# Optimization experiments

Measured on AMD Instinct MI355X. Metric: run time of the kernel, lower is better.

Reference implementation:

```python
import jax, jax.numpy as jnp
import numpy as np

DIM, SEQ, HEADS = 1024, 2048, 8
HEAD_DIM = DIM // HEADS


def setup_inputs() -> dict:
    key = jax.random.key(0)
    ks = jax.random.split(key, 8)
    x = jax.random.normal(ks[0], (4, SEQ, DIM), dtype=jnp.float32)
    # Linear weights stored [in, out]; y = x @ W + b (same math as torch Linear).
    Wk = jax.random.normal(ks[1], (DIM, DIM), dtype=jnp.float32) * (DIM ** -0.5)
    bk = jnp.zeros((DIM,), dtype=jnp.float32)
    Wv = jax.random.normal(ks[2], (DIM, DIM), dtype=jnp.float32) * (DIM ** -0.5)
    bv = jnp.zeros((DIM,), dtype=jnp.float32)
    # learned AFT position bias [heads, seq, seq]; small scale keeps exp stable
    w_aft = jax.random.normal(ks[3], (HEADS, SEQ, SEQ), dtype=jnp.float32) * 0.1
    Wo = jax.random.normal(ks[4], (DIM, DIM), dtype=jnp.float32) * (DIM ** -0.5)
    bo = jnp.zeros((DIM,), dtype=jnp.float32)
    return {"x": x, "Wk": Wk, "bk": bk, "Wv": Wv, "bv": bv,
            "w_aft": w_aft, "Wo": Wo, "bo": bo}


def reference(x, Wk, bk, Wv, bv, w_aft, Wo, bo):
    N, S, _ = x.shape
    k = (x @ Wk + bk).reshape(N, S, HEADS, HEAD_DIM)
    v = (x @ Wv + bv).reshape(N, S, HEADS, HEAD_DIM)
    ek = jnp.exp(k)  # [N,S,H,D]
    # causal mask: position t attends to i <= t; exp(w+k) = exp(w)*exp(k)
    causal = jnp.tril(jnp.ones((S, S), dtype=bool))
    ew = jnp.where(causal[None, :, :], jnp.exp(w_aft), 0.0)  # [H,T,S]
    num = jnp.einsum('hts,nshd->nthd', ew, ek * v)  # [N,T,H,D]
    den = jnp.einsum('hts,nshd->nthd', ew, ek)      # [N,T,H,D]
    aft = (num / den).reshape(N, S, DIM)
    return aft @ Wo + bo
```

## Files before the change

### kernel.cpp

```cpp
#include <hip/hip_runtime.h>
#include <hip/hip_bf16.h>
#include <stdint.h>

#define DIM 1024
#define SEQ 2048
#define NB 4
#define HEADS 8
#define HD 128
#define ROWS (NB*SEQ)

typedef __attribute__((ext_vector_type(8))) short bf16x8;
typedef __attribute__((ext_vector_type(4))) float f32x4;

#define VMCNT(n) asm volatile("s_waitcnt vmcnt(" #n ")" ::: "memory")
#define SBAR()   __builtin_amdgcn_s_barrier()
#define SCHED0() __builtin_amdgcn_sched_barrier(0)

static __device__ __forceinline__ unsigned short f2bf(float f){
  union { float f; unsigned int u; } x; x.f = f;
  unsigned int r = x.u + 0x7fffu + ((x.u >> 16) & 1u);
  return (unsigned short)(r >> 16);
}

static __device__ __forceinline__ void gld_lds16(const void* g, void* l){
  __builtin_amdgcn_global_load_lds(
      (const __attribute__((address_space(1))) void*)g,
      (__attribute__((address_space(3))) void*)l,
      16, 0, 0);
}

__global__ void k_prep(const float* __restrict__ x,
                       const float* __restrict__ Wk, const float* __restrict__ Wv,
                       const float* __restrict__ Wo, const float* __restrict__ waft,
                       unsigned short* __restrict__ xb,
                       unsigned short* __restrict__ Tk, unsigned short* __restrict__ Tv,
                       unsigned short* __restrict__ To, unsigned short* __restrict__ ewb){
  __shared__ float tile[64][65];
  const int B = blockIdx.x;
  const int tid = threadIdx.x;
  if (B < 2048){
    for (int i = B*256 + tid; i < ROWS*DIM/4; i += 2048*256){
      const float4 v = reinterpret_cast<const float4*>(x)[i];
      ushort4 o;
      o.x = f2bf(v.x); o.y = f2bf(v.y); o.z = f2bf(v.z); o.w = f2bf(v.w);
      reinterpret_cast<ushort4*>(xb)[i] = o;
    }
  } else if (B < 2816){
    const int D = B - 2048;
    const int z = D >> 8;
    const int rem = D & 255;
    const int bo = (rem & 15) * 64;
    const int bi = (rem >> 4) * 64;
    const float* W = (z == 0) ? Wk : (z == 1) ? Wv : Wo;
    unsigned short* WT = (z == 0) ? Tk : (z == 1) ? Tv : To;
    #pragma unroll
    for (int it = 0; it < 16; ++it){
      int f = it*256 + tid;
      int r = f >> 6, c = f & 63;
      tile[r][c] = W[(size_t)(bi + r) * DIM + bo + c];
    }
    __syncthreads();
    #pragma unroll
    for (int it = 0; it < 16; ++it){
      int f = it*256 + tid;
      int r = f >> 6, c = f & 63;
      WT[(size_t)(bo + r) * DIM + bi + c] = f2bf(tile[c][r]);
    }
  } else {
    const int D = B - 2816;
    const int t = D & 2047;
    const int h = D >> 11;
    const float* src = waft + ((size_t)h*SEQ + t) * SEQ;
    unsigned short* dst = ewb + ((size_t)h*SEQ + t) * SEQ;
    const int smax4 = ((t & ~127) + 128) >> 2;
    for (int i = tid; i < smax4; i += 256){
      const float4 w4 = reinterpret_cast<const float4*>(src)[i];
      const int s = i * 4;
      ushort4 o;
      o.x = (s+0 <= t) ? f2bf(__expf(w4.x)) : (unsigned short)0;
      o.y = (s+1 <= t) ? f2bf(__expf(w4.y)) : (unsigned short)0;
      o.z = (s+2 <= t) ? f2bf(__expf(w4.z)) : (unsigned short)0;
      o.w = (s+3 <= t) ? f2bf(__expf(w4.w)) : (unsigned short)0;
      reinterpret_cast<ushort4*>(dst)[i] = o;
    }
  }
}

__global__ __launch_bounds__(512) void k_proj(
    const unsigned short* __restrict__ xb,
    const unsigned short* __restrict__ wkt,
    const unsigned short* __restrict__ wvt,
    const float* __restrict__ bk,
    const float* __restrict__ bv,
    unsigned short* __restrict__ ekb)
{
  __shared__ __align__(16) char smem[131072];
  unsigned short* Asl = (unsigned short*)smem;
  unsigned short* Bsl = (unsigned short*)(smem + 65536);
  float* xch = (float*)smem;

  const int tid  = threadIdx.x;
  const int lane = tid & 63;
  const int lo   = lane & 15;
  const int hi   = lane >> 4;
  const int wid  = tid >> 6;
  const int wm   = wid >> 2;
  const int wn   = wid & 3;
  const int D    = blockIdx.x;
  const int mb   = D >> 3;
  const int cb   = D & 7;
  const int row0 = mb * 256;
  const int col0k = cb * 128;

  f32x4 acc[8][4] = {};

  auto stage_unit = [&](int kt, int slot, int u){
    const int half = u & 1;
    const bool isB = (u >> 1) != 0;
    unsigned short* lb = (isB ? Bsl : Asl) + slot*(256*64) + half*(128*64);
    const unsigned short* gb;
    if (!isB)           gb = xb  + (size_t)(row0 + half*128)*DIM + kt*64;
    else if (half == 0) gb = wkt + (size_t)col0k*DIM + kt*64;
    else                gb = wvt + (size_t)col0k*DIM + kt*64;
    #pragma unroll
    for (int it = 0; it < 2; ++it){
      const int po = (it*512 + tid)*16;
      const int r  = po >> 7;
      const int k2 = (po & 127) ^ ((r & 7) << 4);
      gld_lds16(gb + (size_t)r*DIM + (k2 >> 1), (char*)lb + po);
    }
  };

  #pragma unroll
  for (int u = 0; u < 4; ++u) stage_unit(0, 0, u);

  for (int t = 0; t < 16; ++t){
    const int s = t & 1;
    const char* Ab = (const char*)(Asl + s*(256*64));
    const char* Bb = (const char*)(Bsl + s*(256*64));
    #pragma unroll
    for (int q = 0; q < 4; ++q){
      if (t + 1 < 16) stage_unit(t + 1, s ^ 1, q);
      if (q == 0){
        if (t + 1 < 16) { VMCNT(2); } else { VMCNT(0); }
      }
      SCHED0();
      SBAR();
      SCHED0();
      bf16x8 a[2][2], b[4][2];
      #pragma unroll
      for (int mf = 0; mf < 2; ++mf){
        const int R = wm*128 + (q*2 + mf)*16 + lo;
        #pragma unroll
        for (int ks = 0; ks < 2; ++ks){
          const int K2 = (ks*64 + hi*16) ^ ((R & 7) << 4);
          a[mf][ks] = *reinterpret_cast<const bf16x8*>(Ab + R*128 + K2);
        }
      }
      #pragma unroll
      for (int nf = 0; nf < 4; ++nf){
        const int R = wn*64 + nf*16 + lo;
        #pragma unroll
        for (int ks = 0; ks < 2; ++ks){
          const int K2 = (ks*64 + hi*16) ^ ((R & 7) << 4);
          b[nf][ks] = *reinterpret_cast<const bf16x8*>(Bb + R*128 + K2);
        }
      }
      __builtin_amdgcn_s_setprio(1);
      #pragma unroll
      for (int ks = 0; ks < 2; ++ks)
        #pragma unroll
        for (int mf = 0; mf < 2; ++mf)
          #pragma unroll
          for (int nf = 0; nf < 4; ++nf)
            acc[q*2+mf][nf] = __builtin_amdgcn_mfma_f32_16x16x32_bf16(
                a[mf][ks], b[nf][ks], acc[q*2+mf][nf], 0, 0, 0);
      __builtin_amdgcn_s_setprio(0);
      SCHED0();
      SBAR();
    }
  }

  __syncthreads();
  if (wn >= 2){
    #pragma unroll
    for (int mf = 0; mf < 8; ++mf){
      const int rloc = wm*128 + mf*16 + hi*4;
      #pragma unroll
      for (int nf = 0; nf < 4; ++nf){
        const int cv = (wn - 2)*64 + nf*16 + lo;
        #pragma unroll
        for (int jj = 0; jj < 4; ++jj)
          xch[(size_t)(rloc + jj)*128 + cv] = acc[mf][nf][jj];
      }
    }
  }
  __syncthreads();
  if (wn < 2){
    #pragma unroll
    for (int nf = 0; nf < 4; ++nf){
      const int ck = wn*64 + nf*16 + lo;
      const int c  = col0k + ck;
      const int h  = c >> 7;
      const int d  = c & 127;
      const float bkc = bk[c];
      const float bvc = bv[c];
      #pragma unroll
      for (int mf = 0; mf < 8; ++mf){
        const int rloc = wm*128 + mf*16 + hi*4;
        const int r = row0 + rloc;
        const int n = r >> 11;
        const int sidx = r & 2047;
        ushort4 pk, pv;
        #pragma unroll
        for (int jj = 0; jj < 4; ++jj){
          const float kval = acc[mf][nf][jj] + bkc;
          const float vval = xch[(size_t)(rloc + jj)*128 + ck] + bvc;
          const float ek = __expf(kval);
          ((unsigned short*)&pk)[jj] = f2bf(ek);
          ((unsigned short*)&pv)[jj] = f2bf(ek * vval);
        }
        const size_t idx = ((size_t)h*1024 + n*256 + d) * SEQ + sidx;
        *reinterpret_cast<ushort4*>(&ekb[idx]) = pk;
        *reinterpret_cast<ushort4*>(&ekb[idx + (size_t)128*SEQ]) = pv;
      }
    }
  }
}

__global__ __launch_bounds__(512) void k_core(
    const unsigned short* __restrict__ ewb,
    const unsigned short* __restrict__ ekb,
    unsigned short* __restrict__ aftb)
{
  __shared__ __align__(16) char smem[98304];
  unsigned short* Asl = (unsigned short*)smem;
  unsigned short* Bsl = (unsigned short*)(smem + 32768);
  float* xch = (float*)smem;

  const int tid  = threadIdx.x;
  const int lane = tid & 63;
  const int lo   = lane & 15;
  const int hi   = lane >> 4;
  const int wid  = tid >> 6;
  const int wm   = wid >> 2;
  const int wn   = wid & 3;
  const int D  = blockIdx.x;
  const int h  = D & 7;
  const int r_ = D >> 3;
  const int p  = r_ >> 2;
  const int n  = r_ & 3;

  const unsigned short* slab = ekb + ((size_t)h*1024 + n*256) * SEQ;

  #pragma unroll
  for (int half = 0; half < 2; ++half){
    const int tt = half ? p : (15 - p);
    const int t0 = tt * 128;
    const int nst = 2*tt + 2;
    const unsigned short* abase = ewb + ((size_t)h*SEQ + t0) * SEQ;

    f32x4 acc[4][4] = {};

    auto stage_unit = [&](int st, int slot, int u){
      const int s0 = st * 64;
      const int po = tid * 16;
      const int r  = po >> 7;
      const int k2 = (po & 127) ^ ((r & 7) << 4);
      if (u < 2){
        unsigned short* lb = Asl + slot*(128*64) + u*(64*64);
        gld_lds16(abase + (size_t)(u*64 + r)*SEQ + s0 + (k2 >> 1), (char*)lb + po);
      } else {
        unsigned short* lb = Bsl + slot*(256*64) + (u-2)*(64*64);
        gld_lds16(slab + (size_t)((u-2)*64 + r)*SEQ + s0 + (k2 >> 1), (char*)lb + po);
      }
    };

    #pragma unroll
    for (int u = 0; u < 6; ++u) stage_unit(0, 0, u);

    for (int t = 0; t < nst; ++t){
      const int s = t & 1;
      const char* Ab = (const char*)(Asl + s*(128*64));
      const char* Bb = (const char*)(Bsl + s*(256*64));
      #pragma unroll
      for (int q = 0; q < 4; ++q){
        if (q < 3 && t + 1 < nst){
          stage_unit(t + 1, s ^ 1, q*2);
          stage_unit(t + 1, s ^ 1, q*2 + 1);
        }
        if (q == 0){
          if (t + 1 < nst) { VMCNT(2); } else { VMCNT(0); }
        }
        SCHED0();
        SBAR();
        SCHED0();
        bf16x8 a[2], b[4][2];
        {
          const int R = wm*64 + q*16 + lo;
          #pragma unroll
          for (int ks = 0; ks < 2; ++ks){
            const int K2 = (ks*64 + hi*16) ^ ((R & 7) << 4);
            a[ks] = *reinterpret_cast<const bf16x8*>(Ab + R*128 + K2);
          }
        }
        #pragma unroll
        for (int nf = 0; nf < 4; ++nf){
          const int R = wn*64 + nf*16 + lo;
          #pragma unroll
          for (int ks = 0; ks < 2; ++ks){
            const int K2 = (ks*64 + hi*16) ^ ((R & 7) << 4);
            b[nf][ks] = *reinterpret_cast<const bf16x8*>(Bb + R*128 + K2);
          }
        }
        __builtin_amdgcn_s_setprio(1);
        #pragma unroll
        for (int ks = 0; ks < 2; ++ks)
          #pragma unroll
          for (int nf = 0; nf < 4; ++nf)
            acc[q][nf] = __builtin_amdgcn_mfma_f32_16x16x32_bf16(
                a[ks], b[nf][ks], acc[q][nf], 0, 0, 0);
        __builtin_amdgcn_s_setprio(0);
        SCHED0();
        SBAR();
      }
    }

    __syncthreads();
    if (wn >= 2){
      #pragma unroll
      for (int mf = 0; mf < 4; ++mf){
        const int rloc = wm*64 + mf*16 + hi*4;
        #pragma unroll
        for (int nf = 0; nf < 4; ++nf){
          const int dv = (wn - 2)*64 + nf*16 + lo;
          #pragma unroll
          for (int jj = 0; jj < 4; ++jj)
            xch[(size_t)(rloc + jj)*129 + dv] = acc[mf][nf][jj];
        }
      }
    }
    __syncthreads();
    if (wn < 2){
      #pragma unroll
      for (int nf = 0; nf < 4; ++nf){
        const int d = wn*64 + nf*16 + lo;
        #pragma unroll
        for (int mf = 0; mf < 4; ++mf){
          const int rloc = wm*64 + mf*16 + hi*4;
          #pragma unroll
          for (int jj = 0; jj < 4; ++jj){
            const int t = t0 + rloc + jj;
            const float num = xch[(size_t)(rloc + jj)*129 + d];
            aftb[((size_t)n*SEQ + t)*DIM + h*HD + d] = f2bf(num / acc[mf][nf][jj]);
          }
        }
      }
    }
    __syncthreads();
  }
}

__global__ __launch_bounds__(512) void k_out(
    const unsigned short* __restrict__ aftb,
    const unsigned short* __restrict__ wot,
    const float* __restrict__ bo,
    float* __restrict__ out)
{
  __shared__ __align__(16) char smem[98304];
  unsigned short* Asl = (unsigned short*)smem;
  unsigned short* Bsl = (unsigned short*)(smem + 32768);

  const int tid  = threadIdx.x;
  const int lane = tid & 63;
  const int lo   = lane & 15;
  const int hi   = lane >> 4;
  const int wid  = tid >> 6;
  const int wm   = wid >> 2;
  const int wn   = wid & 3;
  const int D    = blockIdx.x;
  const int row0 = (D >> 2) * 128;
  const int col0 = (D & 3) * 256;

  f32x4 acc[4][4] = {};

  auto stage_unit = [&](int kt, int slot, int u){
    const int po = tid * 16;
    const int r  = po >> 7;
    const int k2 = (po & 127) ^ ((r & 7) << 4);
    if (u < 2){
      unsigned short* lb = Asl + slot*(128*64) + u*(64*64);
      gld_lds16(aftb + (size_t)(row0 + u*64 + r)*DIM + kt*64 + (k2 >> 1), (char*)lb + po);
    } else {
      unsigned short* lb = Bsl + slot*(256*64) + (u-2)*(64*64);
      gld_lds16(wot + (size_t)(col0 + (u-2)*64 + r)*DIM + kt*64 + (k2 >> 1), (char*)lb + po);
    }
  };

  #pragma unroll
  for (int u = 0; u < 6; ++u) stage_unit(0, 0, u);

  for (int t = 0; t < 16; ++t){
    const int s = t & 1;
    const char* Ab = (const char*)(Asl + s*(128*64));
    const char* Bb = (const char*)(Bsl + s*(256*64));
    #pragma unroll
    for (int q = 0; q < 4; ++q){
      if (q < 3 && t + 1 < 16){
        stage_unit(t + 1, s ^ 1, q*2);
        stage_unit(t + 1, s ^ 1, q*2 + 1);
      }
      if (q == 0){
        if (t + 1 < 16) { VMCNT(2); } else { VMCNT(0); }
      }
      SCHED0();
      SBAR();
      SCHED0();
      bf16x8 a[2], b[4][2];
      {
        const int R = wm*64 + q*16 + lo;
        #pragma unroll
        for (int ks = 0; ks < 2; ++ks){
          const int K2 = (ks*64 + hi*16) ^ ((R & 7) << 4);
          a[ks] = *reinterpret_cast<const bf16x8*>(Ab + R*128 + K2);
        }
      }
      #pragma unroll
      for (int nf = 0; nf < 4; ++nf){
        const int R = wn*64 + nf*16 + lo;
        #pragma unroll
        for (int ks = 0; ks < 2; ++ks){
          const int K2 = (ks*64 + hi*16) ^ ((R & 7) << 4);
          b[nf][ks] = *reinterpret_cast<const bf16x8*>(Bb + R*128 + K2);
        }
      }
      __builtin_amdgcn_s_setprio(1);
      #pragma unroll
      for (int ks = 0; ks < 2; ++ks)
        #pragma unroll
        for (int nf = 0; nf < 4; ++nf)
          acc[q][nf] = __builtin_amdgcn_mfma_f32_16x16x32_bf16(
              a[ks], b[nf][ks], acc[q][nf], 0, 0, 0);
      __builtin_amdgcn_s_setprio(0);
      SCHED0();
      SBAR();
    }
  }

  #pragma unroll
  for (int nf = 0; nf < 4; ++nf){
    const int c = col0 + wn*64 + nf*16 + lo;
    const float boc = bo[c];
    #pragma unroll
    for (int mf = 0; mf < 4; ++mf){
      #pragma unroll
      for (int jj = 0; jj < 4; ++jj){
        const int r = row0 + wm*64 + mf*16 + hi*4 + jj;
        out[(size_t)r*DIM + c] = acc[mf][nf][jj] + boc;
      }
    }
  }
}

extern "C" void kernel_launch(void* const* d_in, const int* in_sizes, int n_in,
                              void* d_out, int out_size, void* d_ws, size_t ws_size,
                              hipStream_t stream){
  const float* x    = (const float*)d_in[0];
  const float* Wk   = (const float*)d_in[1];
  const float* bk   = (const float*)d_in[2];
  const float* Wv   = (const float*)d_in[3];
  const float* bv   = (const float*)d_in[4];
  const float* waft = (const float*)d_in[5];
  const float* Wo   = (const float*)d_in[6];
  const float* bo   = (const float*)d_in[7];
  float* out = (float*)d_out;

  char* w = (char*)d_ws;
  unsigned short* xb   = (unsigned short*)w; w += (size_t)ROWS*DIM*2;
  unsigned short* wkt  = (unsigned short*)w; w += (size_t)DIM*DIM*2;
  unsigned short* wvt  = (unsigned short*)w; w += (size_t)DIM*DIM*2;
  unsigned short* wot  = (unsigned short*)w; w += (size_t)DIM*DIM*2;
  unsigned short* ekb  = (unsigned short*)w; w += (size_t)HEADS*1024*SEQ*2;
  unsigned short* aftb = (unsigned short*)w; w += (size_t)ROWS*DIM*2;
  unsigned short* ewb  = (unsigned short*)w; w += (size_t)HEADS*SEQ*SEQ*2;

  k_prep<<<19200, 256, 0, stream>>>(x, Wk, Wv, Wo, waft, xb, wkt, wvt, wot, ewb);
  k_proj<<<256, 512, 0, stream>>>(xb, wkt, wvt, bk, bv, ekb);
  k_core<<<256, 512, 0, stream>>>(ewb, ekb, aftb);
  k_out<<<256, 512, 0, stream>>>(aftb, wot, bo, out);
}
```

Measured before the change: 158.1 us.

## Overlap exp(w_aft) conversion with K/V projection GEMM and halve its LDS tile

Moves the masked exp/bf16 conversion of the position bias out of the prep kernel into extra blocks of the projection kernel. The memory-bound conversion can then run alongside the compute-bound K/V GEMM. To make room, the GEMM's K-tile is halved to 32 with LDS cut to 64KB, so two blocks can share a CU. The cost is twice as many k-steps and barriers, plus a two-pass epilogue exchange. The bias blocks still loop serially over 64 rows each, which could leave a tail.

Result: slower. 201.7 us (+27.5%).

```diff
diff --git a/kernel.cpp b/kernel.cpp
--- a/kernel.cpp
+++ b/kernel.cpp
@@ -29,12 +29,12 @@
       16, 0, 0);
 }
 
-__global__ void k_prep(const float* __restrict__ x,
-                       const float* __restrict__ Wk, const float* __restrict__ Wv,
-                       const float* __restrict__ Wo, const float* __restrict__ waft,
-                       unsigned short* __restrict__ xb,
-                       unsigned short* __restrict__ Tk, unsigned short* __restrict__ Tv,
-                       unsigned short* __restrict__ To, unsigned short* __restrict__ ewb){
+__global__ void k_prep0(const float* __restrict__ x,
+                        const float* __restrict__ Wk, const float* __restrict__ Wv,
+                        const float* __restrict__ Wo,
+                        unsigned short* __restrict__ xb,
+                        unsigned short* __restrict__ Tk, unsigned short* __restrict__ Tv,
+                        unsigned short* __restrict__ To){
   __shared__ float tile[64][65];
   const int B = blockIdx.x;
   const int tid = threadIdx.x;
@@ -45,7 +45,7 @@
       o.x = f2bf(v.x); o.y = f2bf(v.y); o.z = f2bf(v.z); o.w = f2bf(v.w);
       reinterpret_cast<ushort4*>(xb)[i] = o;
     }
-  } else if (B < 2816){
+  } else {
     const int D = B - 2048;
     const int z = D >> 8;
     const int rem = D & 255;
@@ -66,37 +66,46 @@
       int r = f >> 6, c = f & 63;
       WT[(size_t)(bo + r) * DIM + bi + c] = f2bf(tile[c][r]);
     }
-  } else {
-    const int D = B - 2816;
-    const int t = D & 2047;
-    const int h = D >> 11;
-    const float* src = waft + ((size_t)h*SEQ + t) * SEQ;
-    unsigned short* dst = ewb + ((size_t)h*SEQ + t) * SEQ;
-    const int smax4 = ((t & ~127) + 128) >> 2;
-    for (int i = tid; i < smax4; i += 256){
-      const float4 w4 = reinterpret_cast<const float4*>(src)[i];
-      const int s = i * 4;
-      ushort4 o;
-      o.x = (s+0 <= t) ? f2bf(__expf(w4.x)) : (unsigned short)0;
-      o.y = (s+1 <= t) ? f2bf(__expf(w4.y)) : (unsigned short)0;
-      o.z = (s+2 <= t) ? f2bf(__expf(w4.z)) : (unsigned short)0;
-      o.w = (s+3 <= t) ? f2bf(__expf(w4.w)) : (unsigned short)0;
-      reinterpret_cast<ushort4*>(dst)[i] = o;
-    }
-  }
-}
-
-__global__ __launch_bounds__(512) void k_proj(
+  }
+}
+
+__global__ __launch_bounds__(512) void k_projew(
     const unsigned short* __restrict__ xb,
     const unsigned short* __restrict__ wkt,
     const unsigned short* __restrict__ wvt,
     const float* __restrict__ bk,
     const float* __restrict__ bv,
-    unsigned short* __restrict__ ekb)
+    const float* __restrict__ waft,
+    unsigned short* __restrict__ ekb,
+    unsigned short* __restrict__ ewb)
 {
-  __shared__ __align__(16) char smem[131072];
+  __shared__ __align__(16) char smem[65536];
+
+  if (blockIdx.x >= 256){
+    const int base = (blockIdx.x - 256) * 64;
+    for (int rr = 0; rr < 64; ++rr){
+      const int row = base + rr;
+      const int t = row & 2047;
+      const int h = row >> 11;
+      const float* src = waft + ((size_t)h*SEQ + t) * SEQ;
+      unsigned short* dst = ewb + ((size_t)h*SEQ + t) * SEQ;
+      const int smax4 = ((t & ~127) + 128) >> 2;
+      for (int i = threadIdx.x; i < smax4; i += 512){
+        const float4 w4 = reinterpret_cast<const float4*>(src)[i];
+        const int s = i * 4;
+        ushort4 o;
+        o.x = (s+0 <= t) ? f2bf(__expf(w4.x)) : (unsigned short)0;
+        o.y = (s+1 <= t) ? f2bf(__expf(w4.y)) : (unsigned short)0;
+        o.z = (s+2 <= t) ? f2bf(__expf(w4.z)) : (unsigned short)0;
+        o.w = (s+3 <= t) ? f2bf(__expf(w4.w)) : (unsigned short)0;
+        reinterpret_cast<ushort4*>(dst)[i] = o;
+      }
+    }
+    return;
+  }
+
   unsigned short* Asl = (unsigned short*)smem;
-  unsigned short* Bsl = (unsigned short*)(smem + 65536);
+  unsigned short* Bsl = (unsigned short*)(smem + 32768);
   float* xch = (float*)smem;
 
   const int tid  = threadIdx.x;
@@ -107,122 +116,114 @@
   const int wm   = wid >> 2;
   const int wn   = wid & 3;
   const int D    = blockIdx.x;
-  const int mb   = D >> 3;
-  const int cb   = D & 7;
-  const int row0 = mb * 256;
-  const int col0k = cb * 128;
+  const int row0 = (D >> 3) * 256;
+  const int col0k = (D & 7) * 128;
 
   f32x4 acc[8][4] = {};
 
   auto stage_unit = [&](int kt, int slot, int u){
-    const int half = u & 1;
-    const bool isB = (u >> 1) != 0;
-    unsigned short* lb = (isB ? Bsl : Asl) + slot*(256*64) + half*(128*64);
-    const unsigned short* gb;
-    if (!isB)           gb = xb  + (size_t)(row0 + half*128)*DIM + kt*64;
-    else if (half == 0) gb = wkt + (size_t)col0k*DIM + kt*64;
-    else                gb = wvt + (size_t)col0k*DIM + kt*64;
-    #pragma unroll
-    for (int it = 0; it < 2; ++it){
-      const int po = (it*512 + tid)*16;
-      const int r  = po >> 7;
-      const int k2 = (po & 127) ^ ((r & 7) << 4);
-      gld_lds16(gb + (size_t)r*DIM + (k2 >> 1), (char*)lb + po);
+    const int po   = tid * 16;
+    const int rloc = (po >> 7) + (u & 1) * 64;
+    const int cg   = (po & 127) ^ ((rloc & 7) << 4);
+    const int half = cg >> 6;
+    const int kb   = cg & 63;
+    if (u < 2){
+      const unsigned short* src = xb + (size_t)(row0 + half*128 + rloc)*DIM + kt*32 + (kb >> 1);
+      gld_lds16(src, (char*)Asl + slot*16384 + (u & 1)*8192 + po);
+    } else {
+      const unsigned short* wsrc = half ? wvt : wkt;
+      const unsigned short* src = wsrc + (size_t)(col0k + rloc)*DIM + kt*32 + (kb >> 1);
+      gld_lds16(src, (char*)Bsl + slot*16384 + (u & 1)*8192 + po);
     }
   };
 
   #pragma unroll
   for (int u = 0; u < 4; ++u) stage_unit(0, 0, u);
 
-  for (int t = 0; t < 16; ++t){
+  for (int t = 0; t < 32; ++t){
     const int s = t & 1;
-    const char* Ab = (const char*)(Asl + s*(256*64));
-    const char* Bb = (const char*)(Bsl + s*(256*64));
+    const char* Ab = (const char*)Asl + s*16384;
+    const char* Bb = (const char*)Bsl + s*16384;
     #pragma unroll
     for (int q = 0; q < 4; ++q){
-      if (t + 1 < 16) stage_unit(t + 1, s ^ 1, q);
+      if (t + 1 < 32) stage_unit(t + 1, s ^ 1, q);
       if (q == 0){
-        if (t + 1 < 16) { VMCNT(2); } else { VMCNT(0); }
+        if (t + 1 < 32) { VMCNT(1); } else { VMCNT(0); }
       }
       SCHED0();
       SBAR();
       SCHED0();
-      bf16x8 a[2][2], b[4][2];
-      #pragma unroll
-      for (int mf = 0; mf < 2; ++mf){
-        const int R = wm*128 + (q*2 + mf)*16 + lo;
-        #pragma unroll
-        for (int ks = 0; ks < 2; ++ks){
-          const int K2 = (ks*64 + hi*16) ^ ((R & 7) << 4);
-          a[mf][ks] = *reinterpret_cast<const bf16x8*>(Ab + R*128 + K2);
-        }
+      bf16x8 a[2], b[4];
+      #pragma unroll
+      for (int mf2 = 0; mf2 < 2; ++mf2){
+        const int rp = (q*2 + mf2)*16 + lo;
+        a[mf2] = *reinterpret_cast<const bf16x8*>(
+            Ab + rp*128 + ((wm*64 + hi*16) ^ ((rp & 7) << 4)));
       }
       #pragma unroll
       for (int nf = 0; nf < 4; ++nf){
-        const int R = wn*64 + nf*16 + lo;
-        #pragma unroll
-        for (int ks = 0; ks < 2; ++ks){
-          const int K2 = (ks*64 + hi*16) ^ ((R & 7) << 4);
-          b[nf][ks] = *reinterpret_cast<const bf16x8*>(Bb + R*128 + K2);
-        }
+        const int rp = (wn & 1)*64 + nf*16 + lo;
+        b[nf] = *reinterpret_cast<const bf16x8*>(
+            Bb + rp*128 + (((wn >> 1)*64 + hi*16) ^ ((rp & 7) << 4)));
       }
       __builtin_amdgcn_s_setprio(1);
       #pragma unroll
-      for (int ks = 0; ks < 2; ++ks)
-        #pragma unroll
-        for (int mf = 0; mf < 2; ++mf)
-          #pragma unroll
-          for (int nf = 0; nf < 4; ++nf)
-            acc[q*2+mf][nf] = __builtin_amdgcn_mfma_f32_16x16x32_bf16(
-                a[mf][ks], b[nf][ks], acc[q*2+mf][nf], 0, 0, 0);
+      for (int mf2 = 0; mf2 < 2; ++mf2)
+        #pragma unroll
+        for (int nf = 0; nf < 4; ++nf)
+          acc[q*2+mf2][nf] = __builtin_amdgcn_mfma_f32_16x16x32_bf16(
+              a[mf2], b[nf], acc[q*2+mf2][nf], 0, 0, 0);
       __builtin_amdgcn_s_setprio(0);
       SCHED0();
       SBAR();
     }
   }
 
-  __syncthreads();
-  if (wn >= 2){
-    #pragma unroll
-    for (int mf = 0; mf < 8; ++mf){
-      const int rloc = wm*128 + mf*16 + hi*4;
-      #pragma unroll
-      for (int nf = 0; nf < 4; ++nf){
-        const int cv = (wn - 2)*64 + nf*16 + lo;
-        #pragma unroll
-        for (int jj = 0; jj < 4; ++jj)
-          xch[(size_t)(rloc + jj)*128 + cv] = acc[mf][nf][jj];
-      }
-    }
-  }
-  __syncthreads();
-  if (wn < 2){
-    #pragma unroll
-    for (int nf = 0; nf < 4; ++nf){
-      const int ck = wn*64 + nf*16 + lo;
-      const int c  = col0k + ck;
-      const int h  = c >> 7;
-      const int d  = c & 127;
-      const float bkc = bk[c];
-      const float bvc = bv[c];
+  #pragma unroll
+  for (int e = 0; e < 2; ++e){
+    __syncthreads();
+    if (wn == 2 + e){
       #pragma unroll
       for (int mf = 0; mf < 8; ++mf){
         const int rloc = wm*128 + mf*16 + hi*4;
-        const int r = row0 + rloc;
-        const int n = r >> 11;
-        const int sidx = r & 2047;
-        ushort4 pk, pv;
-        #pragma unroll
-        for (int jj = 0; jj < 4; ++jj){
-          const float kval = acc[mf][nf][jj] + bkc;
-          const float vval = xch[(size_t)(rloc + jj)*128 + ck] + bvc;
-          const float ek = __expf(kval);
-          ((unsigned short*)&pk)[jj] = f2bf(ek);
-          ((unsigned short*)&pv)[jj] = f2bf(ek * vval);
-        }
-        const size_t idx = ((size_t)h*1024 + n*256 + d) * SEQ + sidx;
-        *reinterpret_cast<ushort4*>(&ekb[idx]) = pk;
-        *reinterpret_cast<ushort4*>(&ekb[idx + (size_t)128*SEQ]) = pv;
+        #pragma unroll
+        for (int nf = 0; nf < 4; ++nf){
+          const int cv = nf*16 + lo;
+          #pragma unroll
+          for (int jj = 0; jj < 4; ++jj)
+            xch[(size_t)(rloc + jj)*64 + cv] = acc[mf][nf][jj];
+        }
+      }
+    }
+    __syncthreads();
+    if (wn == e){
+      #pragma unroll
+      for (int nf = 0; nf < 4; ++nf){
+        const int ck = nf*16 + lo;
+        const int c  = col0k + wn*64 + ck;
+        const int h  = c >> 7;
+        const int d  = c & 127;
+        const float bkc = bk[c];
+        const float bvc = bv[c];
+        #pragma unroll
+        for (int mf = 0; mf < 8; ++mf){
+          const int rloc = wm*128 + mf*16 + hi*4;
+          const int r = row0 + rloc;
+          const int n = r >> 11;
+          const int sidx = r & 2047;
+          ushort4 pk, pv;
+          #pragma unroll
+          for (int jj = 0; jj < 4; ++jj){
+            const float kval = acc[mf][nf][jj] + bkc;
+            const float vval = xch[(size_t)(rloc + jj)*64 + ck] + bvc;
+            const float ek = __expf(kval);
+            ((unsigned short*)&pk)[jj] = f2bf(ek);
+            ((unsigned short*)&pv)[jj] = f2bf(ek * vval);
+          }
+          const size_t idx = ((size_t)h*1024 + n*256 + d) * SEQ + sidx;
+          *reinterpret_cast<ushort4*>(&ekb[idx]) = pk;
+          *reinterpret_cast<ushort4*>(&ekb[idx + (size_t)128*SEQ]) = pv;
+        }
       }
     }
   }
@@ -484,8 +485,8 @@
   unsigned short* aftb = (unsigned short*)w; w += (size_t)ROWS*DIM*2;
   unsigned short* ewb  = (unsigned short*)w; w += (size_t)HEADS*SEQ*SEQ*2;
 
-  k_prep<<<19200, 256, 0, stream>>>(x, Wk, Wv, Wo, waft, xb, wkt, wvt, wot, ewb);
-  k_proj<<<256, 512, 0, stream>>>(xb, wkt, wvt, bk, bv, ekb);
+  k_prep0<<<2816, 256, 0, stream>>>(x, Wk, Wv, Wo, xb, wkt, wvt, wot);
+  k_projew<<<512, 512, 0, stream>>>(xb, wkt, wvt, bk, bv, waft, ekb, ewb);
   k_core<<<256, 512, 0, stream>>>(ewb, ekb, aftb);
   k_out<<<256, 512, 0, stream>>>(aftb, wot, bo, out);
 }
```

## Fuse fp32-to-bf16 conversion of x into projection GEMM A-tile staging

Applied to the files above, without the earlier changes.

Removes the separate x conversion pass from the prep kernel. The projection kernel now loads fp32 x into registers, converts it to bf16 and writes it to LDS in the swizzled layout, while B tiles still use direct global-to-LDS loads. This saves a full write and re-read of the bf16 copy of x, but doubles the A-tile global traffic inside the GEMM, adds register pressure, and turns A staging into a register round trip with extra waits.

Result: slower. 169.9 us (+7.5%).

```diff
diff --git a/kernel.cpp b/kernel.cpp
--- a/kernel.cpp
+++ b/kernel.cpp
@@ -13,6 +13,7 @@
 typedef __attribute__((ext_vector_type(4))) float f32x4;
 
 #define VMCNT(n) asm volatile("s_waitcnt vmcnt(" #n ")" ::: "memory")
+#define LGKM0()  asm volatile("s_waitcnt lgkmcnt(0)" ::: "memory")
 #define SBAR()   __builtin_amdgcn_s_barrier()
 #define SCHED0() __builtin_amdgcn_sched_barrier(0)
 
@@ -29,26 +30,16 @@
       16, 0, 0);
 }
 
-__global__ void k_prep(const float* __restrict__ x,
-                       const float* __restrict__ Wk, const float* __restrict__ Wv,
+__global__ void k_prep(const float* __restrict__ Wk, const float* __restrict__ Wv,
                        const float* __restrict__ Wo, const float* __restrict__ waft,
-                       unsigned short* __restrict__ xb,
                        unsigned short* __restrict__ Tk, unsigned short* __restrict__ Tv,
                        unsigned short* __restrict__ To, unsigned short* __restrict__ ewb){
   __shared__ float tile[64][65];
   const int B = blockIdx.x;
   const int tid = threadIdx.x;
-  if (B < 2048){
-    for (int i = B*256 + tid; i < ROWS*DIM/4; i += 2048*256){
-      const float4 v = reinterpret_cast<const float4*>(x)[i];
-      ushort4 o;
-      o.x = f2bf(v.x); o.y = f2bf(v.y); o.z = f2bf(v.z); o.w = f2bf(v.w);
-      reinterpret_cast<ushort4*>(xb)[i] = o;
-    }
-  } else if (B < 2816){
-    const int D = B - 2048;
-    const int z = D >> 8;
-    const int rem = D & 255;
+  if (B < 768){
+    const int z = B >> 8;
+    const int rem = B & 255;
     const int bo = (rem & 15) * 64;
     const int bi = (rem >> 4) * 64;
     const float* W = (z == 0) ? Wk : (z == 1) ? Wv : Wo;
@@ -67,7 +58,7 @@
       WT[(size_t)(bo + r) * DIM + bi + c] = f2bf(tile[c][r]);
     }
   } else {
-    const int D = B - 2816;
+    const int D = B - 768;
     const int t = D & 2047;
     const int h = D >> 11;
     const float* src = waft + ((size_t)h*SEQ + t) * SEQ;
@@ -87,7 +78,7 @@
 }
 
 __global__ __launch_bounds__(512) void k_proj(
-    const unsigned short* __restrict__ xb,
+    const float* __restrict__ xf,
     const unsigned short* __restrict__ wkt,
     const unsigned short* __restrict__ wvt,
     const float* __restrict__ bk,
@@ -107,21 +98,42 @@
   const int wm   = wid >> 2;
   const int wn   = wid & 3;
   const int D    = blockIdx.x;
-  const int mb   = D >> 3;
-  const int cb   = D & 7;
-  const int row0 = mb * 256;
-  const int col0k = cb * 128;
+  const int row0 = (D >> 3) * 256;
+  const int col0k = (D & 7) * 128;
 
   f32x4 acc[8][4] = {};
-
-  auto stage_unit = [&](int kt, int slot, int u){
-    const int half = u & 1;
-    const bool isB = (u >> 1) != 0;
-    unsigned short* lb = (isB ? Bsl : Asl) + slot*(256*64) + half*(128*64);
-    const unsigned short* gb;
-    if (!isB)           gb = xb  + (size_t)(row0 + half*128)*DIM + kt*64;
-    else if (half == 0) gb = wkt + (size_t)col0k*DIM + kt*64;
-    else                gb = wvt + (size_t)col0k*DIM + kt*64;
+  float4 rA[2][2][2];
+
+  auto issueA = [&](int kt, int half){
+    #pragma unroll
+    for (int it = 0; it < 2; ++it){
+      const int po = (it*512 + tid)*16;
+      const int r  = po >> 7;
+      const int k2 = (po & 127) ^ ((r & 7) << 4);
+      const float* src = xf + (size_t)(row0 + half*128 + r)*DIM + kt*64 + (k2 >> 1);
+      rA[half][it][0] = *reinterpret_cast<const float4*>(src);
+      rA[half][it][1] = *reinterpret_cast<const float4*>(src + 4);
+    }
+  };
+  auto writeA = [&](int slot){
+    #pragma unroll
+    for (int half = 0; half < 2; ++half)
+      #pragma unroll
+      for (int it = 0; it < 2; ++it){
+        const int po = (it*512 + tid)*16;
+        bf16x8 pk;
+        const float* f0 = (const float*)&rA[half][it][0];
+        #pragma unroll
+        for (int j = 0; j < 4; ++j) ((unsigned short*)&pk)[j] = f2bf(f0[j]);
+        const float* f1 = (const float*)&rA[half][it][1];
+        #pragma unroll
+        for (int j = 0; j < 4; ++j) ((unsigned short*)&pk)[4+j] = f2bf(f1[j]);
+        *reinterpret_cast<bf16x8*>((char*)Asl + slot*32768 + half*16384 + po) = pk;
+      }
+  };
+  auto stageB = [&](int kt, int slot, int v){
+    unsigned short* lb = Bsl + slot*(256*64) + v*(128*64);
+    const unsigned short* gb = (v == 0 ? wkt : wvt) + (size_t)col0k*DIM + kt*64;
     #pragma unroll
     for (int it = 0; it < 2; ++it){
       const int po = (it*512 + tid)*16;
@@ -131,18 +143,35 @@
     }
   };
 
-  #pragma unroll
-  for (int u = 0; u < 4; ++u) stage_unit(0, 0, u);
+  issueA(0, 0); issueA(0, 1);
+  stageB(0, 0, 0); stageB(0, 0, 1);
+  VMCNT(4);
+  SCHED0();
+  writeA(0);
+  LGKM0();
+  SCHED0();
 
   for (int t = 0; t < 16; ++t){
     const int s = t & 1;
-    const char* Ab = (const char*)(Asl + s*(256*64));
-    const char* Bb = (const char*)(Bsl + s*(256*64));
+    const bool nxt = (t + 1 < 16);
+    const char* Ab = (const char*)Asl + s*32768;
+    const char* Bb = (const char*)Bsl + s*32768;
     #pragma unroll
     for (int q = 0; q < 4; ++q){
-      if (t + 1 < 16) stage_unit(t + 1, s ^ 1, q);
       if (q == 0){
-        if (t + 1 < 16) { VMCNT(2); } else { VMCNT(0); }
+        if (nxt){ issueA(t + 1, 0); VMCNT(4); } else { VMCNT(0); }
+      } else if (q == 1){
+        if (nxt) issueA(t + 1, 1);
+      } else if (q == 2){
+        if (nxt) stageB(t + 1, s ^ 1, 0);
+      } else {
+        if (nxt){
+          stageB(t + 1, s ^ 1, 1);
+          VMCNT(4);
+          SCHED0();
+          writeA(s ^ 1);
+          LGKM0();
+        }
       }
       SCHED0();
       SBAR();
@@ -476,7 +505,6 @@
   float* out = (float*)d_out;
 
   char* w = (char*)d_ws;
-  unsigned short* xb   = (unsigned short*)w; w += (size_t)ROWS*DIM*2;
   unsigned short* wkt  = (unsigned short*)w; w += (size_t)DIM*DIM*2;
   unsigned short* wvt  = (unsigned short*)w; w += (size_t)DIM*DIM*2;
   unsigned short* wot  = (unsigned short*)w; w += (size_t)DIM*DIM*2;
@@ -484,8 +512,8 @@
   unsigned short* aftb = (unsigned short*)w; w += (size_t)ROWS*DIM*2;
   unsigned short* ewb  = (unsigned short*)w; w += (size_t)HEADS*SEQ*SEQ*2;
 
-  k_prep<<<19200, 256, 0, stream>>>(x, Wk, Wv, Wo, waft, xb, wkt, wvt, wot, ewb);
-  k_proj<<<256, 512, 0, stream>>>(xb, wkt, wvt, bk, bv, ekb);
+  k_prep<<<17152, 256, 0, stream>>>(Wk, Wv, Wo, waft, wkt, wvt, wot, ewb);
+  k_proj<<<256, 512, 0, stream>>>(x, wkt, wvt, bk, bv, ekb);
   k_core<<<256, 512, 0, stream>>>(ewb, ekb, aftb);
   k_out<<<256, 512, 0, stream>>>(aftb, wot, bo, out);
 }
```
